# Kernel tuning notes

Hardware: AMD Instinct MI355X
Metric: run time of the kernel (lower is better)

## Reference

```python
import jax, jax.numpy as jnp
import numpy as np

D_MODEL = 1024
HEADS = 16
D_K = D_MODEL // HEADS


def setup_inputs() -> dict:
    key = jax.random.key(0)
    ks = jax.random.split(key, 12)
    B, S = 2, 2048
    scale = 1.0 / np.sqrt(D_MODEL)
    inp = {
        "q": jax.random.normal(ks[0], (B, S, D_MODEL), dtype=jnp.float32),
        "k": jax.random.normal(ks[1], (B, S, D_MODEL), dtype=jnp.float32),
        "v": jax.random.normal(ks[2], (B, S, D_MODEL), dtype=jnp.float32),
        "src_mask": jax.random.randint(ks[3], (B, 1, S), 0, 2, dtype=jnp.int32),
        # projection params (nn.Linear: y = x @ W.T + b); store W already transposed
        "Wq": jax.random.normal(ks[4], (D_MODEL, D_MODEL), dtype=jnp.float32) * scale,
        "bq": jnp.zeros((D_MODEL,), dtype=jnp.float32),
        "Wk": jax.random.normal(ks[5], (D_MODEL, D_MODEL), dtype=jnp.float32) * scale,
        "bk": jnp.zeros((D_MODEL,), dtype=jnp.float32),
        "Wv": jax.random.normal(ks[6], (D_MODEL, D_MODEL), dtype=jnp.float32) * scale,
        "bv": jnp.zeros((D_MODEL,), dtype=jnp.float32),
        "Wo": jax.random.normal(ks[7], (D_MODEL, D_MODEL), dtype=jnp.float32) * scale,
        "bo": jnp.zeros((D_MODEL,), dtype=jnp.float32),
    }
    return inp


def reference(q, k, v, src_mask, Wq, bq, Wk, bk, Wv, bv, Wo, bo):
    B, S, _ = q.shape
    # QKV projections, reshape to (b, heads, seq, d_k)
    def proj(x, W, b):
        y = x @ W + b  # (b, s, d_model)
        return y.reshape(B, S, HEADS, D_K).transpose(0, 2, 1, 3)

    qh = proj(q, Wq, bq)
    kh = proj(k, Wk, bk)
    vh = proj(v, Wv, bv)

    # scaled dot-product attention with padding mask
    scores = jnp.einsum("bhqd,bhkd->bhqk", qh, kh) / jnp.sqrt(jnp.float32(D_K))
    mask = src_mask[:, None, :, :]  # (b,1,1,s), broadcast over heads & query
    scores = jnp.where(mask == 0, jnp.float32(-1e9), scores)
    probs = jax.nn.softmax(scores, axis=-1)
    # dropout is identity in eval mode (reference baseline)
    ctx = jnp.einsum("bhqk,bhkd->bhqd", probs, vh)
    ctx = ctx.transpose(0, 2, 1, 3).reshape(B, S, D_MODEL)
    return ctx @ Wo + bo
```

## Files before the change

kernel.cpp:

```cpp
#include <hip/hip_runtime.h>
#include <hip/hip_bf16.h>

#define DM 1024
#define SL 2048
#define NH 16
#define DK 64

typedef __bf16 bf16;
typedef __bf16 bf16x8 __attribute__((ext_vector_type(8)));
typedef __bf16 bf16x4 __attribute__((ext_vector_type(4)));
typedef float f32x4 __attribute__((ext_vector_type(4)));
typedef float f32x16 __attribute__((ext_vector_type(16)));

__device__ __forceinline__ void gll16(const void* g, void* l) {
  __builtin_amdgcn_global_load_lds(
      (const __attribute__((address_space(1))) unsigned int*)g,
      (__attribute__((address_space(3))) unsigned int*)l, 16, 0, 0);
}

__global__ __launch_bounds__(256) void cvt_x_kernel(
    const float* __restrict__ q, const float* __restrict__ k, const float* __restrict__ v,
    bf16* __restrict__ xq, bf16* __restrict__ xk, bf16* __restrict__ xv) {
  const float* src; bf16* dst;
  if (blockIdx.y == 0)      { src = q; dst = xq; }
  else if (blockIdx.y == 1) { src = k; dst = xk; }
  else                      { src = v; dst = xv; }
  int i = (blockIdx.x * 256 + threadIdx.x) * 8;
  f32x4 a = *(const f32x4*)(src + i);
  f32x4 b = *(const f32x4*)(src + i + 4);
  bf16x8 o;
  o[0]=(bf16)a[0]; o[1]=(bf16)a[1]; o[2]=(bf16)a[2]; o[3]=(bf16)a[3];
  o[4]=(bf16)b[0]; o[5]=(bf16)b[1]; o[6]=(bf16)b[2]; o[7]=(bf16)b[3];
  *(bf16x8*)(dst + i) = o;
}

__global__ __launch_bounds__(256) void cvt_w_kernel(
    const float* __restrict__ W0, const float* __restrict__ W1,
    const float* __restrict__ W2, const float* __restrict__ W3,
    bf16* __restrict__ T0, bf16* __restrict__ T1,
    bf16* __restrict__ T2, bf16* __restrict__ T3) {
  const float* W; bf16* T;
  switch (blockIdx.y) {
    case 0:  W = W0; T = T0; break;
    case 1:  W = W1; T = T1; break;
    case 2:  W = W2; T = T2; break;
    default: W = W3; T = T3; break;
  }
  __shared__ float t[64][65];
  const int tid = threadIdx.x;
  const int tx = blockIdx.x & 15, ty = blockIdx.x >> 4;
  const int cr = tid >> 4, cc = tid & 15;
  #pragma unroll
  for (int rr = 0; rr < 4; ++rr) {
    int row = rr*16 + cr;
    f32x4 val = *(const f32x4*)(W + (ty*64 + row)*DM + tx*64 + cc*4);
    t[row][cc*4+0] = val[0]; t[row][cc*4+1] = val[1];
    t[row][cc*4+2] = val[2]; t[row][cc*4+3] = val[3];
  }
  __syncthreads();
  #pragma unroll
  for (int rr = 0; rr < 4; ++rr) {
    int nrow = rr*16 + cr;
    bf16x4 o;
    o[0] = (bf16)t[cc*4+0][nrow]; o[1] = (bf16)t[cc*4+1][nrow];
    o[2] = (bf16)t[cc*4+2][nrow]; o[3] = (bf16)t[cc*4+3][nrow];
    *(bf16x4*)(T + (tx*64 + nrow)*DM + ty*64 + cc*4) = o;
  }
}

template<int OUT_HEADS>
__device__ __forceinline__ void gemm_core(
    const bf16* __restrict__ A, const bf16* __restrict__ Bt, const float* __restrict__ bias,
    bf16* __restrict__ outH, float* __restrict__ outF) {
  const int mt = blockIdx.x >> 3, nt = blockIdx.x & 7;
  const int m0 = mt*128, n0 = nt*128;
  __shared__ __attribute__((aligned(16))) bf16 As[128*64];
  __shared__ __attribute__((aligned(16))) bf16 Bs[128*64];
  const int tid = threadIdx.x, lane = tid & 63, w = tid >> 6;
  const int wm = w >> 1, wn = w & 1;
  f32x4 acc[4][4];
  #pragma unroll
  for (int x = 0; x < 4; ++x)
    #pragma unroll
    for (int y = 0; y < 4; ++y)
      #pragma unroll
      for (int e = 0; e < 4; ++e) acc[x][y][e] = 0.f;

  for (int kt = 0; kt < 16; ++kt) {
    const int k0 = kt*64;
    __syncthreads();
    #pragma unroll
    for (int i = 0; i < 4; ++i) {
      int idx = (i*4 + w)*64 + lane;
      int r = idx >> 3;
      int s = (idx & 7) ^ (r & 7);
      gll16(A  + (m0 + r)*DM + k0 + s*8, &As[(i*4 + w)*512]);
      gll16(Bt + (n0 + r)*DM + k0 + s*8, &Bs[(i*4 + w)*512]);
    }
    __syncthreads();
    bf16x8 bfr[4][2];
    #pragma unroll
    for (int ni = 0; ni < 4; ++ni) {
      int row = wn*64 + ni*16 + (lane & 15);
      #pragma unroll
      for (int c = 0; c < 2; ++c) {
        int slot = (lane >> 4) + c*4;
        bfr[ni][c] = *(const bf16x8*)&Bs[row*64 + ((slot ^ (row & 7)) << 3)];
      }
    }
    #pragma unroll
    for (int mi = 0; mi < 4; ++mi) {
      int row = wm*64 + mi*16 + (lane & 15);
      bf16x8 a0 = *(const bf16x8*)&As[row*64 + ((((lane >> 4)    ) ^ (row & 7)) << 3)];
      bf16x8 a1 = *(const bf16x8*)&As[row*64 + ((((lane >> 4) + 4) ^ (row & 7)) << 3)];
      #pragma unroll
      for (int ni = 0; ni < 4; ++ni) {
        acc[mi][ni] = __builtin_amdgcn_mfma_f32_16x16x32_bf16(a0, bfr[ni][0], acc[mi][ni], 0, 0, 0);
        acc[mi][ni] = __builtin_amdgcn_mfma_f32_16x16x32_bf16(a1, bfr[ni][1], acc[mi][ni], 0, 0, 0);
      }
    }
  }
  #pragma unroll
  for (int ni = 0; ni < 4; ++ni) {
    int n = n0 + wn*64 + ni*16 + (lane & 15);
    float bv = bias[n];
    #pragma unroll
    for (int mi = 0; mi < 4; ++mi) {
      #pragma unroll
      for (int j = 0; j < 4; ++j) {
        int m = m0 + wm*64 + mi*16 + ((lane >> 4) << 2) + j;
        float val = acc[mi][ni][j] + bv;
        if (OUT_HEADS) {
          int bb = m >> 11, ss = m & 2047, hh = n >> 6, dd = n & 63;
          outH[(((bb << 4) + hh)*SL + ss)*DK + dd] = (bf16)val;
        } else {
          outF[m*DM + n] = val;
        }
      }
    }
  }
}

__global__ __launch_bounds__(256, 2) void proj_gemm_kernel(
    const bf16* XQ, const bf16* XK, const bf16* XV,
    const bf16* WTQp, const bf16* WTKp, const bf16* WTVp,
    const float* bq, const float* bk, const float* bv,
    bf16* QHp, bf16* KHp, bf16* VHp) {
  const bf16 *A, *Bt; const float* bias; bf16* O;
  if (blockIdx.y == 0)      { A = XQ; Bt = WTQp; bias = bq; O = QHp; }
  else if (blockIdx.y == 1) { A = XK; Bt = WTKp; bias = bk; O = KHp; }
  else                      { A = XV; Bt = WTVp; bias = bv; O = VHp; }
  gemm_core<1>(A, Bt, bias, O, nullptr);
}

__global__ __launch_bounds__(256, 2) void out_gemm_kernel(
    const bf16* CTXp, const bf16* WTOp, const float* bo, float* out) {
  gemm_core<0>(CTXp, WTOp, bo, nullptr, out);
}

__global__ __launch_bounds__(256, 2) void attn_kernel(
    const bf16* __restrict__ QHp, const bf16* __restrict__ KHp,
    const bf16* __restrict__ VHp, const int* __restrict__ msk,
    bf16* __restrict__ CTXp) {
  const int bh = blockIdx.y, b = bh >> 4, h = bh & 15;
  const int q0 = blockIdx.x * 128;
  const bf16* Qp = QHp + bh * SL * DK;
  const bf16* Kp = KHp + bh * SL * DK;
  const bf16* Vp = VHp + bh * SL * DK;
  const int* mp = msk + b * SL;
  __shared__ __attribute__((aligned(16))) bf16 Ks[64*64];
  __shared__ __attribute__((aligned(16))) bf16 Vts[64*64];
  __shared__ __attribute__((aligned(16))) bf16 Ps[4][32*64];
  __shared__ __attribute__((aligned(16))) float mAdd[64];
  const int tid = threadIdx.x, lane = tid & 63, w = tid >> 6;
  const int hi = lane >> 5, l5 = lane & 31;
  const float L2E = 1.44269504f;

  bf16x8 qf[4];
  {
    const bf16* qr = Qp + (q0 + w*32 + l5)*DK + hi*8;
    #pragma unroll
    for (int c = 0; c < 4; ++c) qf[c] = *(const bf16x8*)(qr + c*16);
  }
  f32x16 o0, o1;
  #pragma unroll
  for (int e = 0; e < 16; ++e) { o0[e] = 0.f; o1[e] = 0.f; }
  float m_run = -1e30f, l_run = 0.f;

  for (int kt = 0; kt < 32; ++kt) {
    const int k0 = kt*64;
    __syncthreads();
    #pragma unroll
    for (int i = 0; i < 2; ++i) {
      int idx = (i*4 + w)*64 + lane;
      int r = idx >> 3;
      int s = (idx & 7) ^ (r & 7);
      gll16(Kp + (k0 + r)*DK + s*8, &Ks[(i*4 + w)*512]);
    }
    #pragma unroll
    for (int i = 0; i < 2; ++i) {
      int idx = i*256 + tid;
      int key = idx >> 3, dc = idx & 7;
      bf16x8 vv = *(const bf16x8*)(Vp + (k0 + key)*DK + dc*8);
      #pragma unroll
      for (int j = 0; j < 8; ++j) {
        int d = dc*8 + j;
        Vts[d*64 + ((((key >> 3)) ^ (d & 7)) << 3) + (key & 7)] = vv[j];
      }
    }
    if (tid < 64) mAdd[tid] = (mp[k0 + tid] == 0) ? -1.0e9f : 0.0f;
    __syncthreads();

    f32x16 s0, s1;
    #pragma unroll
    for (int e = 0; e < 16; ++e) { s0[e] = 0.f; s1[e] = 0.f; }
    #pragma unroll
    for (int c = 0; c < 4; ++c) {
      int sl = 2*c + hi;
      int r0 = l5, r1 = 32 + l5;
      bf16x8 kf0 = *(const bf16x8*)&Ks[r0*64 + ((sl ^ (r0 & 7)) << 3)];
      bf16x8 kf1 = *(const bf16x8*)&Ks[r1*64 + ((sl ^ (r1 & 7)) << 3)];
      s0 = __builtin_amdgcn_mfma_f32_32x32x16_bf16(kf0, qf[c], s0, 0, 0, 0);
      s1 = __builtin_amdgcn_mfma_f32_32x32x16_bf16(kf1, qf[c], s1, 0, 0, 0);
    }
    float pv_[32];
    float mt = -1e30f;
    #pragma unroll
    for (int half = 0; half < 2; ++half) {
      #pragma unroll
      for (int qd = 0; qd < 4; ++qd) {
        f32x4 ma = *(const f32x4*)&mAdd[half*32 + qd*8 + hi*4];
        #pragma unroll
        for (int j = 0; j < 4; ++j) {
          float val = (half ? s1[qd*4+j] : s0[qd*4+j]) * 0.125f + ma[j];
          pv_[half*16 + qd*4 + j] = val;
          mt = fmaxf(mt, val);
        }
      }
    }
    mt = fmaxf(mt, __shfl_xor(mt, 32));
    float mnew = fmaxf(m_run, mt);
    float sf = exp2f((m_run - mnew) * L2E);
    m_run = mnew;
    float lsum = 0.f;
    #pragma unroll
    for (int t = 0; t < 32; ++t) {
      float p = exp2f((pv_[t] - mnew) * L2E);
      pv_[t] = p; lsum += p;
    }
    lsum += __shfl_xor(lsum, 32);
    l_run = l_run * sf + lsum;
    #pragma unroll
    for (int reg = 0; reg < 16; ++reg) {
      int crow = (reg & 3) + ((reg >> 2) << 3) + (hi << 2);
      float s_ = __shfl(sf, crow);
      o0[reg] *= s_; o1[reg] *= s_;
    }
    #pragma unroll
    for (int half = 0; half < 2; ++half) {
      #pragma unroll
      for (int qd = 0; qd < 4; ++qd) {
        #pragma unroll
        for (int pr = 0; pr < 2; ++pr) {
          int key = half*32 + qd*8 + hi*4 + pr*2;
          unsigned short ulo = __builtin_bit_cast(unsigned short, (bf16)pv_[half*16 + qd*4 + pr*2]);
          unsigned short uhi = __builtin_bit_cast(unsigned short, (bf16)pv_[half*16 + qd*4 + pr*2 + 1]);
          unsigned pk = (unsigned)ulo | ((unsigned)uhi << 16);
          *(unsigned*)&Ps[w][l5*64 + (((key >> 3) ^ (l5 & 7)) << 3) + (key & 7)] = pk;
        }
      }
    }
    #pragma unroll
    for (int c = 0; c < 4; ++c) {
      int sl = 2*c + hi;
      bf16x8 pa  = *(const bf16x8*)&Ps[w][l5*64 + ((sl ^ (l5 & 7)) << 3)];
      int r0 = l5, r1 = 32 + l5;
      bf16x8 vf0 = *(const bf16x8*)&Vts[r0*64 + ((sl ^ (r0 & 7)) << 3)];
      bf16x8 vf1 = *(const bf16x8*)&Vts[r1*64 + ((sl ^ (r1 & 7)) << 3)];
      o0 = __builtin_amdgcn_mfma_f32_32x32x16_bf16(pa, vf0, o0, 0, 0, 0);
      o1 = __builtin_amdgcn_mfma_f32_32x32x16_bf16(pa, vf1, o1, 0, 0, 0);
    }
  }
  float inv = 1.f / l_run;
  const int sbase = (b * SL) * DM + h * DK;
  #pragma unroll
  for (int reg = 0; reg < 16; ++reg) {
    int crow = (reg & 3) + ((reg >> 2) << 3) + (hi << 2);
    float iv = __shfl(inv, crow);
    int srow = q0 + w*32 + crow;
    CTXp[sbase + srow*DM + l5]      = (bf16)(o0[reg] * iv);
    CTXp[sbase + srow*DM + 32 + l5] = (bf16)(o1[reg] * iv);
  }
}

extern "C" void kernel_launch(void* const* d_in, const int* in_sizes, int n_in,
                              void* d_out, int out_size, void* d_ws, size_t ws_size,
                              hipStream_t stream) {
  const float* q  = (const float*)d_in[0];
  const float* k  = (const float*)d_in[1];
  const float* v  = (const float*)d_in[2];
  const int*  msk = (const int*)d_in[3];
  const float* Wq = (const float*)d_in[4];
  const float* bq = (const float*)d_in[5];
  const float* Wk = (const float*)d_in[6];
  const float* bk = (const float*)d_in[7];
  const float* Wv = (const float*)d_in[8];
  const float* bv = (const float*)d_in[9];
  const float* Wo = (const float*)d_in[10];
  const float* bo = (const float*)d_in[11];
  char* ws = (char*)d_ws;
  bf16* XQ  = (bf16*)(ws + 0);
  bf16* XK  = (bf16*)(ws + 8388608);
  bf16* XV  = (bf16*)(ws + 16777216);
  bf16* WTQ = (bf16*)(ws + 25165824);
  bf16* WTK = (bf16*)(ws + 27262976);
  bf16* WTV = (bf16*)(ws + 29360128);
  bf16* WTO = (bf16*)(ws + 31457280);
  bf16* QHb = (bf16*)(ws + 33554432);
  bf16* KHb = (bf16*)(ws + 41943040);
  bf16* VHb = (bf16*)(ws + 50331648);
  bf16* CTX = (bf16*)(ws + 58720256);
  float* out = (float*)d_out;

  cvt_x_kernel<<<dim3(2048, 3), 256, 0, stream>>>(q, k, v, XQ, XK, XV);
  cvt_w_kernel<<<dim3(256, 4), 256, 0, stream>>>(Wq, Wk, Wv, Wo, WTQ, WTK, WTV, WTO);
  proj_gemm_kernel<<<dim3(256, 3), 256, 0, stream>>>(XQ, XK, XV, WTQ, WTK, WTV,
                                                     bq, bk, bv, QHb, KHb, VHb);
  attn_kernel<<<dim3(16, 32), 256, 0, stream>>>(QHb, KHb, VHb, msk, CTX);
  out_gemm_kernel<<<dim3(256, 1), 256, 0, stream>>>(CTX, WTO, bo, out);
}
```

Baseline: 284.8 us.

## Double-buffer attention K/V, pre-transpose V in projection, keep P in registers

The V projection now writes V already transposed per head, so the attention kernel can stage both K and V^T with async global-to-LDS loads into double buffers and prefetch the next tile while computing the current one. The mask is converted once per block into LDS. The P tile no longer round-trips through shared memory; it is packed to bf16 and exchanged across half-waves with shuffles. The kernel also skips the running-max rescale when the max grows by at most 8, and adds s_setprio around MFMA sections in both attention and GEMM. This trades more LDS (double buffers plus a full-length mask) and extra shuffles for fewer barriers and less LDS traffic.

```diff
diff --git a/kernel.cpp b/kernel.cpp
--- a/kernel.cpp
+++ b/kernel.cpp
@@ -16,6 +16,12 @@
   __builtin_amdgcn_global_load_lds(
       (const __attribute__((address_space(1))) unsigned int*)g,
       (__attribute__((address_space(3))) unsigned int*)l, 16, 0, 0);
+}
+
+__device__ __forceinline__ unsigned pk2(float a, float b) {
+  unsigned short lo = __builtin_bit_cast(unsigned short, (bf16)a);
+  unsigned short hi = __builtin_bit_cast(unsigned short, (bf16)b);
+  return (unsigned)lo | ((unsigned)hi << 16);
 }
 
 __global__ __launch_bounds__(256) void cvt_x_kernel(
@@ -68,7 +74,7 @@
   }
 }
 
-template<int OUT_HEADS>
+template<int MODE>
 __device__ __forceinline__ void gemm_core(
     const bf16* __restrict__ A, const bf16* __restrict__ Bt, const float* __restrict__ bias,
     bf16* __restrict__ outH, float* __restrict__ outF) {
@@ -108,6 +114,7 @@
         bfr[ni][c] = *(const bf16x8*)&Bs[row*64 + ((slot ^ (row & 7)) << 3)];
       }
     }
+    __builtin_amdgcn_s_setprio(1);
     #pragma unroll
     for (int mi = 0; mi < 4; ++mi) {
       int row = wm*64 + mi*16 + (lane & 15);
@@ -119,6 +126,7 @@
         acc[mi][ni] = __builtin_amdgcn_mfma_f32_16x16x32_bf16(a1, bfr[ni][1], acc[mi][ni], 0, 0, 0);
       }
     }
+    __builtin_amdgcn_s_setprio(0);
   }
   #pragma unroll
   for (int ni = 0; ni < 4; ++ni) {
@@ -126,15 +134,24 @@
     float bv = bias[n];
     #pragma unroll
     for (int mi = 0; mi < 4; ++mi) {
-      #pragma unroll
-      for (int j = 0; j < 4; ++j) {
-        int m = m0 + wm*64 + mi*16 + ((lane >> 4) << 2) + j;
-        float val = acc[mi][ni][j] + bv;
-        if (OUT_HEADS) {
-          int bb = m >> 11, ss = m & 2047, hh = n >> 6, dd = n & 63;
-          outH[(((bb << 4) + hh)*SL + ss)*DK + dd] = (bf16)val;
-        } else {
-          outF[m*DM + n] = val;
+      int mb = m0 + wm*64 + mi*16 + ((lane >> 4) << 2);
+      if (MODE == 2) {
+        int bb = mb >> 11, ss = mb & 2047, hh = n >> 6, dd = n & 63;
+        bf16x4 o;
+        #pragma unroll
+        for (int j = 0; j < 4; ++j) o[j] = (bf16)(acc[mi][ni][j] + bv);
+        *(bf16x4*)&outH[(((bb << 4) + hh)*DK + dd)*SL + ss] = o;
+      } else {
+        #pragma unroll
+        for (int j = 0; j < 4; ++j) {
+          int m = mb + j;
+          float val = acc[mi][ni][j] + bv;
+          if (MODE == 1) {
+            int bb = m >> 11, ss = m & 2047, hh = n >> 6, dd = n & 63;
+            outH[(((bb << 4) + hh)*SL + ss)*DK + dd] = (bf16)val;
+          } else {
+            outF[m*DM + n] = val;
+          }
         }
       }
     }
@@ -145,12 +162,10 @@
     const bf16* XQ, const bf16* XK, const bf16* XV,
     const bf16* WTQp, const bf16* WTKp, const bf16* WTVp,
     const float* bq, const float* bk, const float* bv,
-    bf16* QHp, bf16* KHp, bf16* VHp) {
-  const bf16 *A, *Bt; const float* bias; bf16* O;
-  if (blockIdx.y == 0)      { A = XQ; Bt = WTQp; bias = bq; O = QHp; }
-  else if (blockIdx.y == 1) { A = XK; Bt = WTKp; bias = bk; O = KHp; }
-  else                      { A = XV; Bt = WTVp; bias = bv; O = VHp; }
-  gemm_core<1>(A, Bt, bias, O, nullptr);
+    bf16* QHp, bf16* KHp, bf16* VTp) {
+  if (blockIdx.y == 0)      gemm_core<1>(XQ, WTQp, bq, QHp, nullptr);
+  else if (blockIdx.y == 1) gemm_core<1>(XK, WTKp, bk, KHp, nullptr);
+  else                      gemm_core<2>(XV, WTVp, bv, VTp, nullptr);
 }
 
 __global__ __launch_bounds__(256, 2) void out_gemm_kernel(
@@ -160,22 +175,27 @@
 
 __global__ __launch_bounds__(256, 2) void attn_kernel(
     const bf16* __restrict__ QHp, const bf16* __restrict__ KHp,
-    const bf16* __restrict__ VHp, const int* __restrict__ msk,
+    const bf16* __restrict__ VTp, const int* __restrict__ msk,
     bf16* __restrict__ CTXp) {
   const int bh = blockIdx.y, b = bh >> 4, h = bh & 15;
   const int q0 = blockIdx.x * 128;
-  const bf16* Qp = QHp + bh * SL * DK;
-  const bf16* Kp = KHp + bh * SL * DK;
-  const bf16* Vp = VHp + bh * SL * DK;
+  const bf16* Qp  = QHp + bh * SL * DK;
+  const bf16* Kp  = KHp + bh * SL * DK;
+  const bf16* Vtp = VTp + bh * SL * DK;
   const int* mp = msk + b * SL;
-  __shared__ __attribute__((aligned(16))) bf16 Ks[64*64];
-  __shared__ __attribute__((aligned(16))) bf16 Vts[64*64];
-  __shared__ __attribute__((aligned(16))) bf16 Ps[4][32*64];
-  __shared__ __attribute__((aligned(16))) float mAdd[64];
+  __shared__ __attribute__((aligned(16))) bf16 Ks[2][64*64];
+  __shared__ __attribute__((aligned(16))) bf16 Vts[2][64*64];
+  __shared__ __attribute__((aligned(16))) float mAddAll[SL];
   const int tid = threadIdx.x, lane = tid & 63, w = tid >> 6;
   const int hi = lane >> 5, l5 = lane & 31;
   const float L2E = 1.44269504f;
 
+  #pragma unroll
+  for (int i = 0; i < 8; ++i) {
+    int idx = i*256 + tid;
+    mAddAll[idx] = (mp[idx] == 0) ? -1.0e9f : 0.0f;
+  }
+
   bf16x8 qf[4];
   {
     const bf16* qr = Qp + (q0 + w*32 + l5)*DK + hi*8;
@@ -187,49 +207,55 @@
   for (int e = 0; e < 16; ++e) { o0[e] = 0.f; o1[e] = 0.f; }
   float m_run = -1e30f, l_run = 0.f;
 
+  #define STAGE(buf, kt_)                                                  \
+    {                                                                      \
+      const int k0s = (kt_)*64;                                            \
+      _Pragma("unroll")                                                    \
+      for (int i = 0; i < 2; ++i) {                                        \
+        int idx = (i*4 + w)*64 + lane;                                     \
+        int r = idx >> 3;                                                  \
+        int s = (idx & 7) ^ (r & 7);                                       \
+        gll16(Kp + (k0s + r)*DK + s*8, &Ks[buf][(i*4 + w)*512]);           \
+      }                                                                    \
+      _Pragma("unroll")                                                    \
+      for (int i = 0; i < 2; ++i) {                                        \
+        int idx = (i*4 + w)*64 + lane;                                     \
+        int r = idx >> 3;                                                  \
+        int s = (idx & 7) ^ (r & 7);                                       \
+        gll16(Vtp + r*SL + k0s + s*8, &Vts[buf][(i*4 + w)*512]);           \
+      }                                                                    \
+    }
+
+  STAGE(0, 0);
+  __syncthreads();
+
   for (int kt = 0; kt < 32; ++kt) {
+    const int cur = kt & 1;
     const int k0 = kt*64;
-    __syncthreads();
-    #pragma unroll
-    for (int i = 0; i < 2; ++i) {
-      int idx = (i*4 + w)*64 + lane;
-      int r = idx >> 3;
-      int s = (idx & 7) ^ (r & 7);
-      gll16(Kp + (k0 + r)*DK + s*8, &Ks[(i*4 + w)*512]);
-    }
-    #pragma unroll
-    for (int i = 0; i < 2; ++i) {
-      int idx = i*256 + tid;
-      int key = idx >> 3, dc = idx & 7;
-      bf16x8 vv = *(const bf16x8*)(Vp + (k0 + key)*DK + dc*8);
-      #pragma unroll
-      for (int j = 0; j < 8; ++j) {
-        int d = dc*8 + j;
-        Vts[d*64 + ((((key >> 3)) ^ (d & 7)) << 3) + (key & 7)] = vv[j];
-      }
-    }
-    if (tid < 64) mAdd[tid] = (mp[k0 + tid] == 0) ? -1.0e9f : 0.0f;
-    __syncthreads();
+    if (kt < 31) STAGE(cur ^ 1, kt + 1);
 
     f32x16 s0, s1;
     #pragma unroll
     for (int e = 0; e < 16; ++e) { s0[e] = 0.f; s1[e] = 0.f; }
+    __builtin_amdgcn_s_setprio(1);
     #pragma unroll
     for (int c = 0; c < 4; ++c) {
       int sl = 2*c + hi;
       int r0 = l5, r1 = 32 + l5;
-      bf16x8 kf0 = *(const bf16x8*)&Ks[r0*64 + ((sl ^ (r0 & 7)) << 3)];
-      bf16x8 kf1 = *(const bf16x8*)&Ks[r1*64 + ((sl ^ (r1 & 7)) << 3)];
+      bf16x8 kf0 = *(const bf16x8*)&Ks[cur][r0*64 + ((sl ^ (r0 & 7)) << 3)];
+      bf16x8 kf1 = *(const bf16x8*)&Ks[cur][r1*64 + ((sl ^ (r1 & 7)) << 3)];
       s0 = __builtin_amdgcn_mfma_f32_32x32x16_bf16(kf0, qf[c], s0, 0, 0, 0);
       s1 = __builtin_amdgcn_mfma_f32_32x32x16_bf16(kf1, qf[c], s1, 0, 0, 0);
     }
+    __builtin_amdgcn_s_setprio(0);
+
     float pv_[32];
     float mt = -1e30f;
     #pragma unroll
     for (int half = 0; half < 2; ++half) {
       #pragma unroll
       for (int qd = 0; qd < 4; ++qd) {
-        f32x4 ma = *(const f32x4*)&mAdd[half*32 + qd*8 + hi*4];
+        f32x4 ma = *(const f32x4*)&mAddAll[k0 + half*32 + qd*8 + hi*4];
         #pragma unroll
         for (int j = 0; j < 4; ++j) {
           float val = (half ? s1[qd*4+j] : s0[qd*4+j]) * 0.125f + ma[j];
@@ -239,48 +265,56 @@
       }
     }
     mt = fmaxf(mt, __shfl_xor(mt, 32));
-    float mnew = fmaxf(m_run, mt);
-    float sf = exp2f((m_run - mnew) * L2E);
-    m_run = mnew;
+    if (!__all(mt - m_run <= 8.0f)) {
+      float mnew = fmaxf(m_run, mt);
+      float sf = exp2f((m_run - mnew) * L2E);
+      #pragma unroll
+      for (int reg = 0; reg < 16; ++reg) {
+        int crow = (reg & 3) + ((reg >> 2) << 3) + (hi << 2);
+        float s_ = __shfl(sf, crow);
+        o0[reg] *= s_; o1[reg] *= s_;
+      }
+      l_run *= sf;
+      m_run = mnew;
+    }
     float lsum = 0.f;
     #pragma unroll
     for (int t = 0; t < 32; ++t) {
-      float p = exp2f((pv_[t] - mnew) * L2E);
+      float p = exp2f((pv_[t] - m_run) * L2E);
       pv_[t] = p; lsum += p;
     }
     lsum += __shfl_xor(lsum, 32);
-    l_run = l_run * sf + lsum;
-    #pragma unroll
-    for (int reg = 0; reg < 16; ++reg) {
-      int crow = (reg & 3) + ((reg >> 2) << 3) + (hi << 2);
-      float s_ = __shfl(sf, crow);
-      o0[reg] *= s_; o1[reg] *= s_;
-    }
-    #pragma unroll
-    for (int half = 0; half < 2; ++half) {
-      #pragma unroll
-      for (int qd = 0; qd < 4; ++qd) {
-        #pragma unroll
-        for (int pr = 0; pr < 2; ++pr) {
-          int key = half*32 + qd*8 + hi*4 + pr*2;
-          unsigned short ulo = __builtin_bit_cast(unsigned short, (bf16)pv_[half*16 + qd*4 + pr*2]);
-          unsigned short uhi = __builtin_bit_cast(unsigned short, (bf16)pv_[half*16 + qd*4 + pr*2 + 1]);
-          unsigned pk = (unsigned)ulo | ((unsigned)uhi << 16);
-          *(unsigned*)&Ps[w][l5*64 + (((key >> 3) ^ (l5 & 7)) << 3) + (key & 7)] = pk;
-        }
-      }
-    }
+    l_run += lsum;
+
     #pragma unroll
     for (int c = 0; c < 4; ++c) {
+      int half_c = c >> 1;
+      int qo = (2*c + hi) & 3;
+      int qx = (2*c + 1 - hi) & 3;
+      int io = half_c*16 + qo*4, ix = half_c*16 + qx*4;
+      unsigned ow0 = pk2(pv_[io],   pv_[io+1]);
+      unsigned ow1 = pk2(pv_[io+2], pv_[io+3]);
+      unsigned xw0 = pk2(pv_[ix],   pv_[ix+1]);
+      unsigned xw1 = pk2(pv_[ix+2], pv_[ix+3]);
+      unsigned yw0 = __shfl_xor(xw0, 32);
+      unsigned yw1 = __shfl_xor(xw1, 32);
+      union { unsigned u[4]; bf16x8 v; } U;
+      U.u[0] = hi ? yw0 : ow0;
+      U.u[1] = hi ? yw1 : ow1;
+      U.u[2] = hi ? ow0 : yw0;
+      U.u[3] = hi ? ow1 : yw1;
       int sl = 2*c + hi;
-      bf16x8 pa  = *(const bf16x8*)&Ps[w][l5*64 + ((sl ^ (l5 & 7)) << 3)];
       int r0 = l5, r1 = 32 + l5;
-      bf16x8 vf0 = *(const bf16x8*)&Vts[r0*64 + ((sl ^ (r0 & 7)) << 3)];
-      bf16x8 vf1 = *(const bf16x8*)&Vts[r1*64 + ((sl ^ (r1 & 7)) << 3)];
-      o0 = __builtin_amdgcn_mfma_f32_32x32x16_bf16(pa, vf0, o0, 0, 0, 0);
-      o1 = __builtin_amdgcn_mfma_f32_32x32x16_bf16(pa, vf1, o1, 0, 0, 0);
-    }
-  }
+      bf16x8 vf0 = *(const bf16x8*)&Vts[cur][r0*64 + ((sl ^ (r0 & 7)) << 3)];
+      bf16x8 vf1 = *(const bf16x8*)&Vts[cur][r1*64 + ((sl ^ (r1 & 7)) << 3)];
+      __builtin_amdgcn_s_setprio(1);
+      o0 = __builtin_amdgcn_mfma_f32_32x32x16_bf16(U.v, vf0, o0, 0, 0, 0);
+      o1 = __builtin_amdgcn_mfma_f32_32x32x16_bf16(U.v, vf1, o1, 0, 0, 0);
+      __builtin_amdgcn_s_setprio(0);
+    }
+    __syncthreads();
+  }
+
   float inv = 1.f / l_run;
   const int sbase = (b * SL) * DM + h * DK;
   #pragma unroll
@@ -291,6 +325,7 @@
     CTXp[sbase + srow*DM + l5]      = (bf16)(o0[reg] * iv);
     CTXp[sbase + srow*DM + 32 + l5] = (bf16)(o1[reg] * iv);
   }
+  #undef STAGE
 }
 
 extern "C" void kernel_launch(void* const* d_in, const int* in_sizes, int n_in,
@@ -318,14 +353,14 @@
   bf16* WTO = (bf16*)(ws + 31457280);
   bf16* QHb = (bf16*)(ws + 33554432);
   bf16* KHb = (bf16*)(ws + 41943040);
-  bf16* VHb = (bf16*)(ws + 50331648);
+  bf16* VTb = (bf16*)(ws + 50331648);
   bf16* CTX = (bf16*)(ws + 58720256);
   float* out = (float*)d_out;
 
   cvt_x_kernel<<<dim3(2048, 3), 256, 0, stream>>>(q, k, v, XQ, XK, XV);
   cvt_w_kernel<<<dim3(256, 4), 256, 0, stream>>>(Wq, Wk, Wv, Wo, WTQ, WTK, WTV, WTO);
   proj_gemm_kernel<<<dim3(256, 3), 256, 0, stream>>>(XQ, XK, XV, WTQ, WTK, WTV,
-                                                     bq, bk, bv, QHb, KHb, VHb);
-  attn_kernel<<<dim3(16, 32), 256, 0, stream>>>(QHb, KHb, VHb, msk, CTX);
+                                                     bq, bk, bv, QHb, KHb, VTb);
+  attn_kernel<<<dim3(16, 32), 256, 0, stream>>>(QHb, KHb, VTb, msk, CTX);
   out_gemm_kernel<<<dim3(256, 1), 256, 0, stream>>>(CTX, WTO, bo, out);
 }
```

Measured after the change: 485.6 us. 70.5% more time.
